# Performance work log

Hardware: AMD Instinct MI355X
Metric: run time of the kernel (lower is better)

## Reference

```python
import jax, jax.numpy as jnp
import numpy as np
import math

B, IN, D, H, DEPTH, E, K = 16384, 128, 512, 8, 3, 8, 2
FF, EH = 4 * D, 256          # ffn width = 4*d_model; expert hidden fixed at 256 in source
EPSILON = 0.1                # forward() default epsilon (exploration mixing)
LN_EPS = 1e-5


def _ln(x, w, b):
    m = x.mean(-1, keepdims=True)
    v = x.var(-1, keepdims=True)  # biased variance, matching nn.LayerNorm
    return (x - m) / jnp.sqrt(v + LN_EPS) * w + b


def setup_inputs() -> dict:
    key = jax.random.key(0)
    ks = jax.random.split(key, 16)
    s = 0.02
    rn = lambda k, shape: jax.random.normal(k, shape, jnp.float32) * s
    return dict(
        x=jax.random.normal(ks[0], (B, IN), jnp.float32),
        embed_w=rn(ks[1], (IN, D)), embed_b=jnp.zeros((D,), jnp.float32),
        ln1_w=jnp.ones((DEPTH, D), jnp.float32), ln1_b=jnp.zeros((DEPTH, D), jnp.float32),
        inproj_w=rn(ks[2], (DEPTH, 3 * D, D)), inproj_b=jnp.zeros((DEPTH, 3 * D), jnp.float32),
        outproj_w=rn(ks[3], (DEPTH, D, D)), outproj_b=jnp.zeros((DEPTH, D), jnp.float32),
        ln2_w=jnp.ones((DEPTH, D), jnp.float32), ln2_b=jnp.zeros((DEPTH, D), jnp.float32),
        ffn_w1=rn(ks[4], (DEPTH, D, FF)), ffn_b1=jnp.zeros((DEPTH, FF), jnp.float32),
        ffn_w2=rn(ks[5], (DEPTH, FF, D)), ffn_b2=jnp.zeros((DEPTH, D), jnp.float32),
        router_w=rn(ks[6], (D, E)), router_b=jnp.zeros((E,), jnp.float32),
        exp_w1=rn(ks[7], (E, D, EH)), exp_b1=jnp.zeros((E, EH), jnp.float32),
        exp_w2=rn(ks[8], (E, EH, D)), exp_b2=jnp.zeros((E, D), jnp.float32),
        head_ln_w=jnp.ones((D,), jnp.float32), head_ln_b=jnp.zeros((D,), jnp.float32),
        head_w=rn(ks[9], (D, 1)), head_b=jnp.zeros((1,), jnp.float32),
    )


def reference(x, embed_w, embed_b, ln1_w, ln1_b, inproj_w, inproj_b,
              outproj_w, outproj_b, ln2_w, ln2_b, ffn_w1, ffn_b1, ffn_w2, ffn_b2,
              router_w, router_b, exp_w1, exp_b1, exp_w2, exp_b2,
              head_ln_w, head_ln_b, head_w, head_b):
    h = x @ embed_w + embed_b                       # [B, D]; unsqueeze(1) -> seq_len == 1
    for l in range(DEPTH):
        g = _ln(h, ln1_w[l], ln1_b[l])
        qkv = g @ inproj_w[l].T + inproj_b[l]       # [B, 3D]
        # seq_len == 1: softmax over the single key is exactly 1, so attn(h,h,h) == out_proj(V)
        v = qkv[:, 2 * D:]
        a = v @ outproj_w[l].T + outproj_b[l]
        h = h + a
        g = _ln(h, ln2_w[l], ln2_b[l])
        h = h + jax.nn.gelu(g @ ffn_w1[l] + ffn_b1[l], approximate=False) @ ffn_w2[l] + ffn_b2[l]
    z = h                                           # squeeze(1)

    # WaggleGate
    logits = z @ router_w + router_b                # [B, E]
    probs = jax.nn.softmax(logits, axis=-1)
    probs = (1.0 - EPSILON) * probs + EPSILON / E
    wts, idx = jax.lax.top_k(probs, K)              # [B, K]
    load = probs.mean(0)
    aux = (load * jnp.log(load * E + 1e-9)).sum() / math.log(E + 1e-9)

    # dense all-expert compute + sparse top-k combine (same math as per-sample dispatch)
    hmid = jax.nn.gelu(jnp.einsum('bd,edh->ebh', z, exp_w1) + exp_b1[:, None, :], approximate=False)
    eo = jnp.einsum('ebh,ehd->ebd', hmid, exp_w2) + exp_b2[:, None, :]   # [E, B, D]
    gate = jnp.zeros((z.shape[0], E), z.dtype).at[
        jnp.arange(z.shape[0])[:, None], idx].add(wts)                    # [B, E]
    moe = jnp.einsum('be,ebd->bd', gate, eo)

    z = z + moe
    logit = (_ln(z, head_ln_w, head_ln_b) @ head_w + head_b)[:, 0]       # [B]
    return logit, aux
```

## Files before the change

### kernel.cpp

```cpp
#include <hip/hip_runtime.h>
#include <hip/hip_bf16.h>

#define B_TOK 16384
#define IN_DIM 128
#define D_DIM 512
#define DEPTH 3
#define NEXP 8
#define FF_DIM 2048
#define EH_DIM 256
#define MAXSLOT 34816
#define MAXT256 136
#define NHBLK 64

typedef __attribute__((ext_vector_type(8))) __bf16 bf16x8;
typedef __attribute__((ext_vector_type(4))) float f32x4;
typedef __attribute__((ext_vector_type(4))) unsigned short u16x4;
typedef __attribute__((ext_vector_type(8))) unsigned short u16x8;

__device__ __forceinline__ unsigned short f2bf(float f){
    unsigned int u = __float_as_uint(f);
    u += 0x7fffu + ((u >> 16) & 1u);
    return (unsigned short)(u >> 16);
}
__device__ __forceinline__ float bf2f(unsigned short u){
    return __uint_as_float(((unsigned int)u) << 16);
}
__device__ __forceinline__ float geluf(float x){
    float x2 = x * x;
    float y  = x * (0.79788456080287f + 0.03567740814183f * x2);
    y = fminf(fmaxf(y, -15.0f), 15.0f);
    float e = __expf(2.0f * y);
    float th = 1.0f - 2.0f / (e + 1.0f);
    return 0.5f * x * (1.0f + th);
}
__device__ __forceinline__ void gload_lds16(const void* g, void* l){
    __builtin_amdgcn_global_load_lds((const __attribute__((address_space(1))) unsigned int*)g,
                                     (__attribute__((address_space(3))) unsigned int*)l,
                                     16, 0, 0);
}
__device__ __forceinline__ int xcd_swizzle(int orig, int nwg){
    const int q = nwg >> 3, r = nwg & 7;
    const int xcd = orig & 7;
    const int idx = orig >> 3;
    return (xcd < r ? xcd*(q+1) : r*(q+1) + (xcd-r)*q) + idx;
}
__device__ __forceinline__ void wgbar(){
    asm volatile("" ::: "memory");
    __builtin_amdgcn_s_barrier();
    asm volatile("" ::: "memory");
}

__global__ void zero_kernel(int* a, int na, int* b, int nb){
    const int i = blockIdx.x * blockDim.x + threadIdx.x;
    if (i < na) a[i] = 0;
    if (i < nb) b[i] = 0;
}

struct ConvSeg { const float* src; unsigned short* dst; int n4; };
struct ConvArgs { ConvSeg seg[2]; };

__global__ void convert_kernel(ConvArgs a){
    const int stride = gridDim.x * blockDim.x;
    const int tid = blockIdx.x * blockDim.x + threadIdx.x;
    for (int s = 0; s < 2; ++s){
        const f32x4* src = (const f32x4*)a.seg[s].src;
        u16x4* dst = (u16x4*)a.seg[s].dst;
        const int n4 = a.seg[s].n4;
        for (int i = tid; i < n4; i += stride){
            f32x4 v = src[i];
            u16x4 o;
            o[0] = f2bf(v[0]); o[1] = f2bf(v[1]); o[2] = f2bf(v[2]); o[3] = f2bf(v[3]);
            dst[i] = o;
        }
    }
}

struct TSeg { const float* src; unsigned short* dst; int K; int N; int tileStart; };
struct TArgs { TSeg seg[26]; };

__global__ void transpose_kernel(TArgs a){
    __shared__ float t[32][33];
    const int tile = blockIdx.x;
    int s = 0;
    #pragma unroll 1
    while (s < 25 && tile >= a.seg[s+1].tileStart) ++s;
    const TSeg sg = a.seg[s];
    const int local = tile - sg.tileStart;
    const int tilesN = sg.N >> 5;
    const int k0 = (local / tilesN) << 5;
    const int n0 = (local % tilesN) << 5;
    const int tx = threadIdx.x & 31;
    const int ty = threadIdx.x >> 5;
    #pragma unroll
    for (int j = 0; j < 4; ++j)
        t[ty + j*8][tx] = sg.src[(size_t)(k0 + ty + j*8) * sg.N + n0 + tx];
    __syncthreads();
    #pragma unroll
    for (int j = 0; j < 4; ++j){
        const int n = ty + j*8;
        sg.dst[(size_t)(n0 + n) * sg.K + k0 + tx] = f2bf(t[tx][n]);
    }
}

__global__ void foldb_kernel(const float* __restrict__ outproj_w, const float* __restrict__ outproj_b,
                             const float* __restrict__ inproj_b, float* __restrict__ bfold){
    const int wave = threadIdx.x >> 6, lane = threadIdx.x & 63;
    const int o = blockIdx.x * 4 + wave;
    const int l = o >> 9, n = o & 511;
    const float* Wo = outproj_w + ((size_t)l*D_DIM + n)*D_DIM;
    const float* bv = inproj_b + l*3*D_DIM + 2*D_DIM;
    float s = 0.f;
    #pragma unroll
    for (int j = 0; j < 8; ++j) s += Wo[lane + j*64] * bv[lane + j*64];
    #pragma unroll
    for (int off = 32; off > 0; off >>= 1) s += __shfl_xor(s, off);
    if (lane == 0) bfold[o] = s + outproj_b[o];
}

__global__ void __launch_bounds__(256, 2)
gemm_bt(const unsigned short* __restrict__ A0, const unsigned short* __restrict__ Bt0,
        const float* __restrict__ bias, unsigned short* __restrict__ out0,
        int NB, int N, int K, int nper, size_t lsa, size_t lsb, size_t lsc)
{
    __shared__ unsigned short sh[32768];
    const int nwg = gridDim.x;
    int wg  = xcd_swizzle(blockIdx.x, nwg);
    const int layer = wg / nper;
    wg -= layer * nper;
    const unsigned short* A  = A0  + (size_t)layer * lsa;
    const unsigned short* Bt = Bt0 + (size_t)layer * lsb;
    unsigned short* out = out0 + (size_t)layer * lsc;
    const int bn  = wg % NB;
    const int bm  = wg / NB;

    const int tid  = threadIdx.x;
    const int lane = tid & 63;
    const int wave = tid >> 6;
    const int wm = (wave >> 1) << 6;
    const int wn = (wave & 1) << 6;

    f32x4 acc[4][4] = {};

    const unsigned short* Abase = A + (size_t)bm * 128 * K;
    const unsigned short* Bbase = Bt + (size_t)bn * 128 * K;
    const int soff = tid * 16;

    auto STAGE = [&](int b, int kt){
        char* Ab = (char*)(sh + b*16384);
        char* Bb = (char*)(sh + b*16384 + 8192);
        #pragma unroll
        for (int s = 0; s < 4; ++s){
            const int off = s*4096 + soff;
            const int row = off >> 7, colb = off & 127;
            gload_lds16((const char*)(Abase + (size_t)row*K + kt) + colb, Ab + off);
        }
        #pragma unroll
        for (int s = 0; s < 4; ++s){
            const int off = s*4096 + soff;
            const int row = off >> 7, colb = off & 127;
            gload_lds16((const char*)(Bbase + (size_t)row*K + kt) + colb, Bb + off);
        }
    };
    auto COMPUTE = [&](int b){
        const unsigned short* Ab = sh + b*16384;
        const unsigned short* Bb = sh + b*16384 + 8192;
        #pragma unroll
        for (int ks = 0; ks < 2; ++ks){
            const int k0 = ks*32 + ((lane>>4)<<3);
            bf16x8 af[4], bfr[4];
            #pragma unroll
            for (int i=0;i<4;i++) af[i]  = *(const bf16x8*)&Ab[(wm + i*16 + (lane&15))*64 + k0];
            #pragma unroll
            for (int j=0;j<4;j++) bfr[j] = *(const bf16x8*)&Bb[(wn + j*16 + (lane&15))*64 + k0];
            #pragma unroll
            for (int i=0;i<4;i++)
                #pragma unroll
                for (int j=0;j<4;j++)
                    acc[i][j] = __builtin_amdgcn_mfma_f32_16x16x32_bf16(af[i], bfr[j], acc[i][j], 0, 0, 0);
        }
    };

    STAGE(0, 0);
    __syncthreads();
    const int nk = K >> 6;
    int cur = 0;
    for (int i = 0; i < nk; ++i){
        if (i + 1 < nk) STAGE(cur ^ 1, (i + 1) << 6);
        COMPUTE(cur);
        __syncthreads();
        cur ^= 1;
    }

    const int r0 = ((lane>>4)<<2);
    const int cc = lane & 15;
    unsigned short* Ct = sh;
    float bcol[4];
    #pragma unroll
    for (int j=0;j<4;j++) bcol[j] = bias[bn*128 + wn + j*16 + cc];
    #pragma unroll
    for (int i=0;i<4;i++)
        #pragma unroll
        for (int r=0;r<4;r++){
            const int rl = wm + i*16 + r0 + r;
            #pragma unroll
            for (int j=0;j<4;j++)
                Ct[rl*128 + wn + j*16 + cc] = f2bf(acc[i][j][r] + bcol[j]);
        }
    __syncthreads();
    const int orow = tid >> 4;
    const int ocol = (tid & 15) * 8;
    #pragma unroll
    for (int p = 0; p < 8; ++p){
        const int row = p*16 + orow;
        *(u16x8*)(&out[(size_t)(bm*128 + row)*N + bn*128 + ocol]) = *(u16x8*)&Ct[row*128 + ocol];
    }
}

__global__ void __launch_bounds__(512, 2)
gemm256sq(const unsigned short* __restrict__ A, const unsigned short* __restrict__ Bt,
          const float* __restrict__ bias, unsigned short* __restrict__ out,
          int NB, int N, int K)
{
    __shared__ __align__(16) char sh[131072];
    const int nwg = gridDim.x;
    const int wg  = xcd_swizzle(blockIdx.x, nwg);
    const int bn  = wg % NB;
    const int bm  = wg / NB;
    const int m0  = bm * 256;
    const int n0  = bn * 256;

    const int tid = threadIdx.x, lane = tid & 63, wave = tid >> 6;
    const int wr = wave >> 2;
    const int wc = wave & 3;

    const int srow8  = tid >> 3;
    const int schunk = (tid & 7) ^ (srow8 & 7);
    const unsigned short* Ab = A  + (size_t)m0 * K + schunk*8;
    const unsigned short* Bb = Bt + (size_t)n0 * K + schunk*8;
    const int ldst = (tid & 7) * 16;

    auto STA = [&](int slot, int half, int kt){
        #pragma unroll
        for (int l = 0; l < 2; ++l){
            const int r = half*128 + srow8 + l*64;
            gload_lds16(Ab + (size_t)r*K + kt, sh + slot*32768 + r*128 + ldst);
        }
    };
    auto STB = [&](int slot, int half, int kt){
        #pragma unroll
        for (int l = 0; l < 2; ++l){
            const int r = half*128 + srow8 + l*64;
            gload_lds16(Bb + (size_t)r*K + kt, sh + 65536 + slot*32768 + r*128 + ldst);
        }
    };

    int ch[2];
    #pragma unroll
    for (int ks = 0; ks < 2; ++ks)
        ch[ks] = ((((ks<<2) + (lane>>4)) ^ (lane & 7)) << 4);
    const int arow = wr*128 + (lane & 15);
    const int brow = wc*64  + (lane & 15);

    f32x4 acc[8][4] = {};
    bf16x8 bfr[4][2];

    auto PHASE = [&](int slot, int mfb, bool rb, auto&& issue, int wait){
        if (rb){
            #pragma unroll
            for (int nf = 0; nf < 4; ++nf)
                #pragma unroll
                for (int ks = 0; ks < 2; ++ks)
                    bfr[nf][ks] = *(const bf16x8*)(sh + 65536 + slot*32768 + (brow + nf*16)*128 + ch[ks]);
        }
        bf16x8 af[2][2];
        #pragma unroll
        for (int m2 = 0; m2 < 2; ++m2)
            #pragma unroll
            for (int ks = 0; ks < 2; ++ks)
                af[m2][ks] = *(const bf16x8*)(sh + slot*32768 + (arow + (mfb+m2)*16)*128 + ch[ks]);
        issue();
        if (wait == 4)      asm volatile("s_waitcnt vmcnt(4)" ::: "memory");
        else if (wait == 0) asm volatile("s_waitcnt vmcnt(0)" ::: "memory");
        wgbar();
        __builtin_amdgcn_s_setprio(1);
        #pragma unroll
        for (int m2 = 0; m2 < 2; ++m2)
            #pragma unroll
            for (int nf = 0; nf < 4; ++nf)
                #pragma unroll
                for (int ks = 0; ks < 2; ++ks)
                    acc[mfb+m2][nf] = __builtin_amdgcn_mfma_f32_16x16x32_bf16(af[m2][ks], bfr[nf][ks], acc[mfb+m2][nf], 0,0,0);
        __builtin_amdgcn_s_setprio(0);
        wgbar();
    };

    STB(0,0,0); STB(0,1,0);
    STA(0,0,0); STA(0,1,0);
    STB(1,0,64); STB(1,1,64);
    asm volatile("s_waitcnt vmcnt(4)" ::: "memory");
    wgbar();

    const int nk = K >> 6;
    const int NT = nk >> 1;
    for (int it = 0; it < NT; ++it){
        const bool mp = (it + 1 < NT);
        const int k1 = (2*it + 1) << 6;
        const int k2 = (2*it + 2) << 6;
        const int k3 = (2*it + 3) << 6;
        PHASE(0, 0, true,  [&]{ STA(1,0,k1); }, -1);
        PHASE(0, 2, false, [&]{ STA(1,1,k1); if (mp) STB(0,0,k2); }, -1);
        PHASE(0, 4, false, [&]{ if (mp) STB(0,1,k2); }, -1);
        PHASE(0, 6, false, [&]{}, mp ? 4 : 0);
        PHASE(1, 0, true,  [&]{ if (mp) STA(0,0,k2); }, -1);
        PHASE(1, 2, false, [&]{ if (mp) STA(0,1,k2); }, -1);
        PHASE(1, 4, false, [&]{ if (mp) STB(1,0,k3); }, -1);
        PHASE(1, 6, false, [&]{ if (mp) STB(1,1,k3); }, mp ? 4 : 0);
    }

    unsigned short* Ct = (unsigned short*)sh;
    const int r4 = (lane >> 4) * 4;
    const int cc = lane & 15;
    #pragma unroll
    for (int nf = 0; nf < 4; ++nf){
        const int col = wc*64 + nf*16 + cc;
        const float bv = bias[n0 + col];
        #pragma unroll
        for (int mf = 0; mf < 8; ++mf)
            #pragma unroll
            for (int r = 0; r < 4; ++r){
                const int row = wr*128 + mf*16 + r4 + r;
                Ct[row*256 + col] = f2bf(geluf(acc[mf][nf][r] + bv));
            }
    }
    __syncthreads();
    #pragma unroll
    for (int p = 0; p < 16; ++p){
        const int uidx = p*512 + tid;
        const int row = uidx >> 5;
        const int cu  = uidx & 31;
        *(u16x8*)(out + (size_t)(m0 + row)*N + n0 + cu*8) = *(const u16x8*)(Ct + row*256 + cu*8);
    }
}

#define G_GELU_BF16 0
#define G_BF16_RESID 1
#define G_GATED_BF16 2

template<int EPI, int MOE, int INDIRECT>
__global__ void __launch_bounds__(512, 2)
gemm256(const unsigned short* __restrict__ A, const unsigned short* __restrict__ BtG,
        const float* __restrict__ biasG, const unsigned short* __restrict__ resid,
        const int* __restrict__ tok, const int* __restrict__ offs,
        int wstride, int bstride, const float* __restrict__ gslot,
        unsigned short* __restrict__ out, int NB, int N, int K)
{
    __shared__ __align__(16) char sh[147456];
    const int nwg = gridDim.x;
    const int wg  = xcd_swizzle(blockIdx.x, nwg);
    const int bn  = wg % NB;
    const int bm  = wg / NB;
    const int m0  = bm * 256;

    const unsigned short* Bt = BtG;
    const float* bias = biasG;
    if (MOE){
        if (m0 >= offs[8]) return;
        int e = 0;
        #pragma unroll 1
        while (offs[e+1] <= m0) ++e;
        Bt   += (size_t)e * wstride;
        bias += (size_t)e * bstride;
    }

    const int tid = threadIdx.x, lane = tid & 63, wave = tid >> 6;
    const int wm = (wave >> 1) * 64;
    const int wn = (wave & 1) * 64;

    const int srow = wave*16 + (lane >> 3);
    const int scol = ((lane & 7) ^ (lane >> 3)) * 8;
    const unsigned short* aptr[2][2];
    #pragma unroll
    for (int u = 0; u < 2; ++u)
        #pragma unroll
        for (int l = 0; l < 2; ++l){
            const int r = u*128 + srow + l*8;
            const int gr = INDIRECT ? tok[m0 + r] : (m0 + r);
            aptr[u][l] = A + (size_t)gr * K + scol;
        }
    const unsigned short* bptr[2];
    #pragma unroll
    for (int l = 0; l < 2; ++l)
        bptr[l] = Bt + (size_t)(bn*128 + srow + l*8) * K + scol;
    const int sdst = wave*2048 + lane*16;

    int aoff[2], boff[2];
    #pragma unroll
    for (int ks = 0; ks < 2; ++ks){
        const int ch = (((ks<<2) + (lane>>4)) ^ (lane & 7)) << 4;
        aoff[ks] = (wm + (lane & 15))*128 + ch;
        boff[ks] = (wn + (lane & 15))*128 + ch;
    }

    f32x4 acc[4][4] = {};

    auto STAGE = [&](int buf, int kt){
        #pragma unroll
        for (int u = 0; u < 2; ++u)
            #pragma unroll
            for (int l = 0; l < 2; ++l)
                gload_lds16(aptr[u][l] + kt, sh + buf*32768 + u*16384 + l*1024 + sdst);
        #pragma unroll
        for (int l = 0; l < 2; ++l)
            gload_lds16(bptr[l] + kt, sh + 98304 + buf*16384 + l*1024 + sdst);
    };
    auto COMPUTE = [&](int buf){
        bf16x8 bfr[4][2];
        #pragma unroll
        for (int nf = 0; nf < 4; ++nf)
            #pragma unroll
            for (int ks = 0; ks < 2; ++ks)
                bfr[nf][ks] = *(const bf16x8*)(sh + 98304 + buf*16384 + nf*2048 + boff[ks]);
        #pragma unroll
        for (int mf = 0; mf < 4; ++mf){
            bf16x8 af[2];
            #pragma unroll
            for (int ks = 0; ks < 2; ++ks)
                af[ks] = *(const bf16x8*)(sh + buf*32768 + mf*2048 + aoff[ks]);
            #pragma unroll
            for (int nf = 0; nf < 4; ++nf)
                #pragma unroll
                for (int ks = 0; ks < 2; ++ks)
                    acc[mf][nf] = __builtin_amdgcn_mfma_f32_16x16x32_bf16(af[ks], bfr[nf][ks], acc[mf][nf], 0,0,0);
        }
    };

    STAGE(0, 0);
    __syncthreads();
    const int nk = K >> 6;
    int cur = 0;
    for (int i = 0; i < nk; ++i){
        if (i + 1 < nk) STAGE(cur ^ 1, (i + 1) << 6);
        COMPUTE(cur);
        __syncthreads();
        cur ^= 1;
    }

    const int r4 = (lane >> 4) * 4;
    const int cc = lane & 15;
    if (EPI == G_BF16_RESID){
        float* ctf = (float*)sh;
        #pragma unroll
        for (int nf = 0; nf < 4; ++nf){
            const float bv = bias[bn*128 + wn + nf*16 + cc];
            #pragma unroll
            for (int mf = 0; mf < 4; ++mf)
                #pragma unroll
                for (int r = 0; r < 4; ++r){
                    const int row = wm + mf*16 + r4 + r;
                    ctf[row*128 + wn + nf*16 + cc] = acc[mf][nf][r] + bv;
                }
        }
        __syncthreads();
        #pragma unroll
        for (int p = 0; p < 8; ++p){
            const int uidx = p*512 + tid;
            const int row = uidx >> 4;
            const int cu  = uidx & 15;
            const size_t gidx = (size_t)(m0 + row)*N + bn*128 + cu*8;
            u16x8 hv = *(const u16x8*)(resid + gidx);
            u16x8 o;
            #pragma unroll
            for (int j = 0; j < 8; ++j)
                o[j] = f2bf(bf2f(hv[j]) + ctf[row*128 + cu*8 + j]);
            *(u16x8*)(out + gidx) = o;
        }
    } else {
        unsigned short* ct = (unsigned short*)sh;
        #pragma unroll
        for (int nf = 0; nf < 4; ++nf){
            const float bv = bias[bn*128 + wn + nf*16 + cc];
            #pragma unroll
            for (int mf = 0; mf < 4; ++mf)
                #pragma unroll
                for (int r = 0; r < 4; ++r){
                    const int row = wm + mf*16 + r4 + r;
                    float v = acc[mf][nf][r] + bv;
                    if (EPI == G_GELU_BF16) v = geluf(v);
                    else                    v *= gslot[m0 + row];
                    ct[row*128 + wn + nf*16 + cc] = f2bf(v);
                }
        }
        __syncthreads();
        #pragma unroll
        for (int p = 0; p < 8; ++p){
            const int uidx = p*512 + tid;
            const int row = uidx >> 4;
            const int cu  = uidx & 15;
            *(u16x8*)(out + (size_t)(m0 + row)*N + bn*128 + cu*8) =
                *(const u16x8*)(ct + row*128 + cu*8);
        }
    }
}

__global__ void ln_kernel(const unsigned short* __restrict__ x, const float* __restrict__ w,
                          const float* __restrict__ b, unsigned short* __restrict__ out)
{
    const int lane = threadIdx.x & 63;
    const int wave = threadIdx.x >> 6;
    const int row  = blockIdx.x * 4 + wave;
    u16x8 hv = *(const u16x8*)(x + (size_t)row * D_DIM + lane*8);
    float v[8];
    #pragma unroll
    for (int j = 0; j < 8; ++j) v[j] = bf2f(hv[j]);
    float s = 0.f, s2 = 0.f;
    #pragma unroll
    for (int j = 0; j < 8; ++j){ s += v[j]; s2 += v[j]*v[j]; }
    #pragma unroll
    for (int o = 32; o > 0; o >>= 1){ s += __shfl_xor(s, o); s2 += __shfl_xor(s2, o); }
    const float mean = s * (1.0f/512.0f);
    const float var  = s2 * (1.0f/512.0f) - mean*mean;
    const float inv  = 1.0f / sqrtf(var + 1e-5f);
    const int k = lane*8;
    u16x8 o;
    #pragma unroll
    for (int j = 0; j < 8; ++j) o[j] = f2bf((v[j]-mean)*inv*w[k+j] + b[k+j]);
    *(u16x8*)(out + (size_t)row*D_DIM + k) = o;
}

__global__ void router_kernel(const unsigned short* __restrict__ z, const float* __restrict__ rw,
                              const float* __restrict__ rb,
                              int2* __restrict__ idx2, float2* __restrict__ wts2,
                              float* __restrict__ bsums)
{
    __shared__ float ps[4][8];
    const int lane = threadIdx.x & 63;
    const int wave = threadIdx.x >> 6;
    const int row  = blockIdx.x * 4 + wave;
    u16x8 hv = *(const u16x8*)(z + (size_t)row * D_DIM + lane*8);
    float acc[8] = {0,0,0,0,0,0,0,0};
    #pragma unroll
    for (int j = 0; j < 8; ++j){
        const float zv = bf2f(hv[j]);
        const float* wr = rw + (size_t)(lane*8 + j) * 8;
        f32x4 w0 = *(const f32x4*)wr;
        f32x4 w1 = *(const f32x4*)(wr + 4);
        acc[0] += zv*w0[0]; acc[1] += zv*w0[1]; acc[2] += zv*w0[2]; acc[3] += zv*w0[3];
        acc[4] += zv*w1[0]; acc[5] += zv*w1[1]; acc[6] += zv*w1[2]; acc[7] += zv*w1[3];
    }
    #pragma unroll
    for (int o = 32; o > 0; o >>= 1){
        #pragma unroll
        for (int e = 0; e < 8; ++e) acc[e] += __shfl_xor(acc[e], o);
    }
    if (lane == 0){
        float p[8]; float mx = -1e30f;
        #pragma unroll
        for (int e=0;e<8;e++){ p[e] = acc[e] + rb[e]; mx = fmaxf(mx, p[e]); }
        float se = 0.f;
        #pragma unroll
        for (int e=0;e<8;e++){ p[e] = expf(p[e]-mx); se += p[e]; }
        const float sc = 0.9f / se;
        #pragma unroll
        for (int e=0;e<8;e++) p[e] = p[e]*sc + 0.0125f;
        int i1 = 0;
        #pragma unroll
        for (int e=1;e<8;e++) if (p[e] > p[i1]) i1 = e;
        int i2 = (i1 == 0) ? 1 : 0;
        for (int e=i2+1;e<8;e++) if (e != i1 && p[e] > p[i2]) i2 = e;
        idx2[row] = make_int2(i1, i2);
        wts2[row] = make_float2(p[i1], p[i2]);
        #pragma unroll
        for (int e=0;e<8;e++) ps[wave][e] = p[e];
    }
    __syncthreads();
    if (threadIdx.x < 8){
        bsums[blockIdx.x*8 + threadIdx.x] =
            ps[0][threadIdx.x] + ps[1][threadIdx.x] + ps[2][threadIdx.x] + ps[3][threadIdx.x];
    }
}

__global__ void hist_kernel(const int2* __restrict__ idx2, int* __restrict__ blockHist){
    __shared__ int hc[8];
    if (threadIdx.x < 8) hc[threadIdx.x] = 0;
    __syncthreads();
    const int t = blockIdx.x * 256 + threadIdx.x;
    const int2 ii = idx2[t];
    atomicAdd(&hc[ii.x], 1);
    atomicAdd(&hc[ii.y], 1);
    __syncthreads();
    if (threadIdx.x < 8) blockHist[blockIdx.x*8 + threadIdx.x] = hc[threadIdx.x];
}

__global__ void scan_kernel(const int* __restrict__ blockHist, int* __restrict__ offs,
                            int* __restrict__ baseArr){
    __shared__ int hist[NHBLK*8];
    __shared__ int cnt[8];
    __shared__ int start[8];
    const int t = threadIdx.x;
    hist[t] = blockHist[t];
    __syncthreads();
    if (t < 8){
        int c = 0;
        #pragma unroll 1
        for (int b = 0; b < NHBLK; ++b) c += hist[b*8 + t];
        cnt[t] = c;
    }
    __syncthreads();
    if (t == 0){
        int o = 0; offs[0] = 0;
        for (int e = 0; e < 8; ++e){ start[e] = o; o += (cnt[e]+255)&~255; offs[e+1] = o; }
    }
    __syncthreads();
    if (t < 8){
        int cur = start[t];
        #pragma unroll 1
        for (int b = 0; b < NHBLK; ++b){ baseArr[b*8 + t] = cur; cur += hist[b*8 + t]; }
    }
}

__global__ void assign_kernel(const int2* __restrict__ idx2, const float2* __restrict__ wts2,
                              const int* __restrict__ baseArr, int2* __restrict__ slot_map,
                              float* __restrict__ gslot, int* __restrict__ tok)
{
    __shared__ int cur[8];
    if (threadIdx.x < 8) cur[threadIdx.x] = 0;
    __syncthreads();
    const int t = blockIdx.x * 256 + threadIdx.x;
    const int2 ii = idx2[t];
    const float2 ww = wts2[t];
    const int r1 = atomicAdd(&cur[ii.x], 1);
    const int r2 = atomicAdd(&cur[ii.y], 1);
    const int s1 = baseArr[blockIdx.x*8 + ii.x] + r1;
    const int s2 = baseArr[blockIdx.x*8 + ii.y] + r2;
    slot_map[t] = make_int2(s1, s2);
    gslot[s1] = ww.x; gslot[s2] = ww.y;
    tok[s1] = t; tok[s2] = t;
}

__global__ void aux_kernel(const float* __restrict__ bsums, float* __restrict__ out_aux)
{
    __shared__ float part[256];
    const int t = threadIdx.x;
    const int e = t & 7, chunk = t >> 3;
    float s = 0.f;
    for (int blk = chunk*128; blk < chunk*128 + 128; ++blk) s += bsums[blk*8 + e];
    part[t] = s;
    __syncthreads();
    if (t < 8){
        float tot = 0.f;
        for (int c = 0; c < 32; ++c) tot += part[c*8 + t];
        part[t] = tot;
    }
    __syncthreads();
    if (t == 0){
        float aux = 0.f;
        for (int e2 = 0; e2 < 8; ++e2){
            float load = part[e2] * (1.0f/16384.0f);
            aux += load * logf(load * 8.0f + 1e-9f);
        }
        out_aux[0] = aux / 2.0794415416798357f;
    }
}

__global__ void head_kernel(const unsigned short* __restrict__ h, const unsigned short* __restrict__ eog,
                            const int2* __restrict__ slot_map,
                            const float* __restrict__ w, const float* __restrict__ b,
                            const float* __restrict__ hw, const float* __restrict__ hb,
                            float* __restrict__ out)
{
    const int lane = threadIdx.x & 63;
    const int wave = threadIdx.x >> 6;
    const int row  = blockIdx.x * 4 + wave;
    const int2 sm = slot_map[row];
    u16x8 hv = *(const u16x8*)(h + (size_t)row * D_DIM + lane*8);
    u16x8 e1 = *(const u16x8*)(eog + (size_t)sm.x * D_DIM + lane*8);
    u16x8 e2 = *(const u16x8*)(eog + (size_t)sm.y * D_DIM + lane*8);
    float v[8];
    #pragma unroll
    for (int j=0;j<8;j++) v[j] = bf2f(hv[j]) + bf2f(e1[j]) + bf2f(e2[j]);
    float s = 0.f, s2 = 0.f;
    #pragma unroll
    for (int j=0;j<8;j++){ s += v[j]; s2 += v[j]*v[j]; }
    #pragma unroll
    for (int o = 32; o > 0; o >>= 1){ s += __shfl_xor(s, o); s2 += __shfl_xor(s2, o); }
    const float mean = s * (1.0f/512.0f);
    const float var  = s2 * (1.0f/512.0f) - mean*mean;
    const float inv  = 1.0f / sqrtf(var + 1e-5f);
    const int k = lane*8;
    float dot = 0.f;
    #pragma unroll
    for (int j=0;j<8;j++) dot += ((v[j]-mean)*inv*w[k+j] + b[k+j]) * hw[k+j];
    #pragma unroll
    for (int o = 32; o > 0; o >>= 1) dot += __shfl_xor(dot, o);
    if (lane == 0) out[row] = dot + hb[0];
}

extern "C" void kernel_launch(void* const* d_in, const int* in_sizes, int n_in,
                              void* d_out, int out_size, void* d_ws, size_t ws_size,
                              hipStream_t stream)
{
    (void)in_sizes; (void)n_in; (void)out_size; (void)ws_size;
    const float* x         = (const float*)d_in[0];
    const float* embed_w   = (const float*)d_in[1];
    const float* embed_b   = (const float*)d_in[2];
    const float* ln1_w     = (const float*)d_in[3];
    const float* ln1_b     = (const float*)d_in[4];
    const float* inproj_w  = (const float*)d_in[5];
    const float* inproj_b  = (const float*)d_in[6];
    const float* outproj_w = (const float*)d_in[7];
    const float* outproj_b = (const float*)d_in[8];
    const float* ln2_w     = (const float*)d_in[9];
    const float* ln2_b     = (const float*)d_in[10];
    const float* ffn_w1    = (const float*)d_in[11];
    const float* ffn_b1    = (const float*)d_in[12];
    const float* ffn_w2    = (const float*)d_in[13];
    const float* ffn_b2    = (const float*)d_in[14];
    const float* router_w  = (const float*)d_in[15];
    const float* router_b  = (const float*)d_in[16];
    const float* exp_w1    = (const float*)d_in[17];
    const float* exp_b1    = (const float*)d_in[18];
    const float* exp_w2    = (const float*)d_in[19];
    const float* exp_b2    = (const float*)d_in[20];
    const float* head_ln_w = (const float*)d_in[21];
    const float* head_ln_b = (const float*)d_in[22];
    const float* head_w    = (const float*)d_in[23];
    const float* head_b    = (const float*)d_in[24];

    char* ws = (char*)d_ws;
    unsigned short* xbf   = (unsigned short*)(ws + 0);
    unsigned short* ebf   = (unsigned short*)(ws + 4194304);
    unsigned short* wobf  = (unsigned short*)(ws + 4325376);
    unsigned short* wvtbf = (unsigned short*)(ws + 5898240);
    unsigned short* wfold = (unsigned short*)(ws + 7471104);
    unsigned short* w1t   = (unsigned short*)(ws + 9043968);
    unsigned short* w2t   = (unsigned short*)(ws + 15335424);
    unsigned short* e1t   = (unsigned short*)(ws + 21626880);
    unsigned short* e2t   = (unsigned short*)(ws + 23724032);
    unsigned short* h     = (unsigned short*)(ws + 25821184);
    unsigned short* gbf   = (unsigned short*)(ws + 42598400);
    unsigned short* ubf   = (unsigned short*)(ws + 59375616);
    unsigned short* hmidg = ubf;
    unsigned short* eog   = (unsigned short*)(ws + 77201408);
    char* MISC = ws + 126484480;
    int*    offs     = (int*)(MISC + 0);
    float*  zbias    = (float*)(MISC + 256);
    float*  bfold    = (float*)(MISC + 2304);
    int2*   idx2     = (int2*)(MISC + 8448);
    float2* wts2     = (float2*)(MISC + 139520);
    int2*   slot_map = (int2*)(MISC + 270592);
    float*  gslot    = (float*)(MISC + 401664);
    int*    tok      = (int*)(MISC + 544768);
    float*  bsums    = (float*)(MISC + 684032);
    int*    blockHist= (int*)(MISC + 815104);
    int*    baseArr  = (int*)(MISC + 817152);
    float* out = (float*)d_out;

    zero_kernel<<<(MAXSLOT + 255)/256, 256, 0, stream>>>((int*)zbias, 512, tok, MAXSLOT);

    ConvArgs ca;
    ca.seg[0] = { x, xbf, B_TOK*IN_DIM/4 };
    ca.seg[1] = { outproj_w, wobf, DEPTH*D_DIM*D_DIM/4 };
    convert_kernel<<<1024, 256, 0, stream>>>(ca);

    TArgs ta;
    int tcur = 0, ti = 0;
    ta.seg[ti] = { embed_w, ebf, IN_DIM, D_DIM, tcur };
    tcur += (IN_DIM/32)*(D_DIM/32); ++ti;
    for (int l = 0; l < DEPTH; ++l){
        ta.seg[ti] = { ffn_w1 + (size_t)l*D_DIM*FF_DIM, w1t + (size_t)l*FF_DIM*D_DIM, D_DIM, FF_DIM, tcur };
        tcur += (D_DIM/32)*(FF_DIM/32); ++ti;
    }
    for (int l = 0; l < DEPTH; ++l){
        ta.seg[ti] = { ffn_w2 + (size_t)l*FF_DIM*D_DIM, w2t + (size_t)l*D_DIM*FF_DIM, FF_DIM, D_DIM, tcur };
        tcur += (FF_DIM/32)*(D_DIM/32); ++ti;
    }
    for (int e = 0; e < NEXP; ++e){
        ta.seg[ti] = { exp_w1 + (size_t)e*D_DIM*EH_DIM, e1t + (size_t)e*EH_DIM*D_DIM, D_DIM, EH_DIM, tcur };
        tcur += (D_DIM/32)*(EH_DIM/32); ++ti;
    }
    for (int e = 0; e < NEXP; ++e){
        ta.seg[ti] = { exp_w2 + (size_t)e*EH_DIM*D_DIM, e2t + (size_t)e*D_DIM*EH_DIM, EH_DIM, D_DIM, tcur };
        tcur += (EH_DIM/32)*(D_DIM/32); ++ti;
    }
    for (int l = 0; l < DEPTH; ++l){
        ta.seg[ti] = { inproj_w + (size_t)l*3*D_DIM*D_DIM + 2*D_DIM*D_DIM,
                       wvtbf + (size_t)l*D_DIM*D_DIM, D_DIM, D_DIM, tcur };
        tcur += (D_DIM/32)*(D_DIM/32); ++ti;
    }
    transpose_kernel<<<tcur, 256, 0, stream>>>(ta);

    foldb_kernel<<<DEPTH*D_DIM/4, 256, 0, stream>>>(outproj_w, outproj_b, inproj_b, bfold);

    gemm_bt<<<48, 256, 0, stream>>>(
        wobf, wvtbf, zbias, wfold, 4, D_DIM, D_DIM,
        16, (size_t)D_DIM*D_DIM, (size_t)D_DIM*D_DIM, (size_t)D_DIM*D_DIM);

    gemm_bt<<<(D_DIM/128)*(B_TOK/128), 256, 0, stream>>>(
        xbf, ebf, embed_b, h, D_DIM/128, D_DIM, IN_DIM,
        (D_DIM/128)*(B_TOK/128), 0, 0, 0);

    for (int l = 0; l < DEPTH; ++l){
        ln_kernel<<<B_TOK/4, 256, 0, stream>>>(h, ln1_w + l*D_DIM, ln1_b + l*D_DIM, gbf);
        gemm256<G_BF16_RESID,0,0><<<(B_TOK/256)*(D_DIM/128), 512, 0, stream>>>(
            gbf, wfold + (size_t)l*D_DIM*D_DIM, bfold + l*D_DIM, h,
            nullptr, nullptr, 0, 0, nullptr, h, D_DIM/128, D_DIM, D_DIM);
        ln_kernel<<<B_TOK/4, 256, 0, stream>>>(h, ln2_w + l*D_DIM, ln2_b + l*D_DIM, gbf);
        gemm256sq<<<(B_TOK/256)*(FF_DIM/256), 512, 0, stream>>>(
            gbf, w1t + (size_t)l*FF_DIM*D_DIM, ffn_b1 + l*FF_DIM, ubf, FF_DIM/256, FF_DIM, D_DIM);
        gemm256<G_BF16_RESID,0,0><<<(B_TOK/256)*(D_DIM/128), 512, 0, stream>>>(
            ubf, w2t + (size_t)l*D_DIM*FF_DIM, ffn_b2 + l*D_DIM, h,
            nullptr, nullptr, 0, 0, nullptr, h, D_DIM/128, D_DIM, FF_DIM);
    }

    router_kernel<<<B_TOK/4, 256, 0, stream>>>(h, router_w, router_b, idx2, wts2, bsums);
    aux_kernel<<<1, 256, 0, stream>>>(bsums, out + B_TOK);
    hist_kernel<<<NHBLK, 256, 0, stream>>>(idx2, blockHist);
    scan_kernel<<<1, 512, 0, stream>>>(blockHist, offs, baseArr);
    assign_kernel<<<B_TOK/256, 256, 0, stream>>>(idx2, wts2, baseArr, slot_map, gslot, tok);

    gemm256<G_GELU_BF16,1,1><<<MAXT256*(EH_DIM/128), 512, 0, stream>>>(
        h, e1t, exp_b1, nullptr, tok, offs, EH_DIM*D_DIM, EH_DIM, nullptr,
        hmidg, EH_DIM/128, EH_DIM, D_DIM);
    gemm256<G_GATED_BF16,1,0><<<MAXT256*(D_DIM/128), 512, 0, stream>>>(
        hmidg, e2t, exp_b2, nullptr, nullptr, offs, D_DIM*EH_DIM, D_DIM, gslot,
        eog, D_DIM/128, D_DIM, EH_DIM);

    head_kernel<<<B_TOK/4, 256, 0, stream>>>(h, eog, slot_map, head_ln_w, head_ln_b, head_w, head_b, out);
}
```

Measured before the change: 571.0 us.

## Halve GEMM K-tile to 32 to cut LDS footprint and raise occupancy

Both the 256x256 GELU GEMM and the generic 256x128 GEMM now stage K-tiles of 32 instead of 64, which shrinks shared memory from 128-144KB to 64KB per workgroup. The 256-square kernel also drops its hand-scheduled eight-phase pipeline with interleaved barriers and priority hints, and uses a plain double-buffered loop. Epilogues are split into two 128-row halves so the output staging fits in the smaller LDS. The aim is more resident workgroups per CU and simpler scheduling, at the cost of twice as many barriers per K and less latency hiding within each workgroup.

```diff
diff --git a/kernel.cpp b/kernel.cpp
--- a/kernel.cpp
+++ b/kernel.cpp
@@ -43,11 +43,6 @@
     const int xcd = orig & 7;
     const int idx = orig >> 3;
     return (xcd < r ? xcd*(q+1) : r*(q+1) + (xcd-r)*q) + idx;
-}
-__device__ __forceinline__ void wgbar(){
-    asm volatile("" ::: "memory");
-    __builtin_amdgcn_s_barrier();
-    asm volatile("" ::: "memory");
 }
 
 __global__ void zero_kernel(int* a, int na, int* b, int nb){
@@ -221,7 +216,7 @@
           const float* __restrict__ bias, unsigned short* __restrict__ out,
           int NB, int N, int K)
 {
-    __shared__ __align__(16) char sh[131072];
+    __shared__ __align__(16) char sh[65536];
     const int nwg = gridDim.x;
     const int wg  = xcd_swizzle(blockIdx.x, nwg);
     const int bn  = wg % NB;
@@ -233,112 +228,86 @@
     const int wr = wave >> 2;
     const int wc = wave & 3;
 
-    const int srow8  = tid >> 3;
-    const int schunk = (tid & 7) ^ (srow8 & 7);
-    const unsigned short* Ab = A  + (size_t)m0 * K + schunk*8;
-    const unsigned short* Bb = Bt + (size_t)n0 * K + schunk*8;
-    const int ldst = (tid & 7) * 16;
-
-    auto STA = [&](int slot, int half, int kt){
-        #pragma unroll
-        for (int l = 0; l < 2; ++l){
-            const int r = half*128 + srow8 + l*64;
-            gload_lds16(Ab + (size_t)r*K + kt, sh + slot*32768 + r*128 + ldst);
-        }
+    const unsigned short* apt[2]; int adst[2];
+    const unsigned short* bpt[2];
+    #pragma unroll
+    for (int l = 0; l < 2; ++l){
+        const int slot = l*512 + tid;
+        const int row = slot >> 2, ch = slot & 3;
+        const int srccol = ((ch ^ (row & 3)) << 3);
+        apt[l]  = A  + (size_t)(m0 + row)*K + srccol;
+        bpt[l]  = Bt + (size_t)(n0 + row)*K + srccol;
+        adst[l] = row*64 + ch*16;
+    }
+    auto STAGE = [&](int buf, int kt){
+        #pragma unroll
+        for (int l = 0; l < 2; ++l)
+            gload_lds16(apt[l] + kt, sh + buf*16384 + adst[l]);
+        #pragma unroll
+        for (int l = 0; l < 2; ++l)
+            gload_lds16(bpt[l] + kt, sh + 32768 + buf*16384 + adst[l]);
     };
-    auto STB = [&](int slot, int half, int kt){
-        #pragma unroll
-        for (int l = 0; l < 2; ++l){
-            const int r = half*128 + srow8 + l*64;
-            gload_lds16(Bb + (size_t)r*K + kt, sh + 65536 + slot*32768 + r*128 + ldst);
-        }
-    };
-
-    int ch[2];
-    #pragma unroll
-    for (int ks = 0; ks < 2; ++ks)
-        ch[ks] = ((((ks<<2) + (lane>>4)) ^ (lane & 7)) << 4);
+
+    const int rch  = (((lane>>4) ^ (lane & 3)) << 4);
     const int arow = wr*128 + (lane & 15);
     const int brow = wc*64  + (lane & 15);
 
     f32x4 acc[8][4] = {};
-    bf16x8 bfr[4][2];
-
-    auto PHASE = [&](int slot, int mfb, bool rb, auto&& issue, int wait){
-        if (rb){
+
+    auto COMPUTE = [&](int buf){
+        bf16x8 bfr[4];
+        #pragma unroll
+        for (int nf = 0; nf < 4; ++nf)
+            bfr[nf] = *(const bf16x8*)(sh + 32768 + buf*16384 + (brow + nf*16)*64 + rch);
+        #pragma unroll
+        for (int mf = 0; mf < 8; ++mf){
+            bf16x8 af = *(const bf16x8*)(sh + buf*16384 + (arow + mf*16)*64 + rch);
             #pragma unroll
             for (int nf = 0; nf < 4; ++nf)
-                #pragma unroll
-                for (int ks = 0; ks < 2; ++ks)
-                    bfr[nf][ks] = *(const bf16x8*)(sh + 65536 + slot*32768 + (brow + nf*16)*128 + ch[ks]);
-        }
-        bf16x8 af[2][2];
-        #pragma unroll
-        for (int m2 = 0; m2 < 2; ++m2)
-            #pragma unroll
-            for (int ks = 0; ks < 2; ++ks)
-                af[m2][ks] = *(const bf16x8*)(sh + slot*32768 + (arow + (mfb+m2)*16)*128 + ch[ks]);
-        issue();
-        if (wait == 4)      asm volatile("s_waitcnt vmcnt(4)" ::: "memory");
-        else if (wait == 0) asm volatile("s_waitcnt vmcnt(0)" ::: "memory");
-        wgbar();
-        __builtin_amdgcn_s_setprio(1);
-        #pragma unroll
-        for (int m2 = 0; m2 < 2; ++m2)
-            #pragma unroll
-            for (int nf = 0; nf < 4; ++nf)
-                #pragma unroll
-                for (int ks = 0; ks < 2; ++ks)
-                    acc[mfb+m2][nf] = __builtin_amdgcn_mfma_f32_16x16x32_bf16(af[m2][ks], bfr[nf][ks], acc[mfb+m2][nf], 0,0,0);
-        __builtin_amdgcn_s_setprio(0);
-        wgbar();
+                acc[mf][nf] = __builtin_amdgcn_mfma_f32_16x16x32_bf16(af, bfr[nf], acc[mf][nf], 0,0,0);
+        }
     };
 
-    STB(0,0,0); STB(0,1,0);
-    STA(0,0,0); STA(0,1,0);
-    STB(1,0,64); STB(1,1,64);
-    asm volatile("s_waitcnt vmcnt(4)" ::: "memory");
-    wgbar();
-
-    const int nk = K >> 6;
-    const int NT = nk >> 1;
-    for (int it = 0; it < NT; ++it){
-        const bool mp = (it + 1 < NT);
-        const int k1 = (2*it + 1) << 6;
-        const int k2 = (2*it + 2) << 6;
-        const int k3 = (2*it + 3) << 6;
-        PHASE(0, 0, true,  [&]{ STA(1,0,k1); }, -1);
-        PHASE(0, 2, false, [&]{ STA(1,1,k1); if (mp) STB(0,0,k2); }, -1);
-        PHASE(0, 4, false, [&]{ if (mp) STB(0,1,k2); }, -1);
-        PHASE(0, 6, false, [&]{}, mp ? 4 : 0);
-        PHASE(1, 0, true,  [&]{ if (mp) STA(0,0,k2); }, -1);
-        PHASE(1, 2, false, [&]{ if (mp) STA(0,1,k2); }, -1);
-        PHASE(1, 4, false, [&]{ if (mp) STB(1,0,k3); }, -1);
-        PHASE(1, 6, false, [&]{ if (mp) STB(1,1,k3); }, mp ? 4 : 0);
+    STAGE(0, 0);
+    __syncthreads();
+    const int nk = K >> 5;
+    int cur = 0;
+    for (int i = 0; i < nk; ++i){
+        if (i + 1 < nk) STAGE(cur ^ 1, (i + 1) << 5);
+        COMPUTE(cur);
+        __syncthreads();
+        cur ^= 1;
     }
 
     unsigned short* Ct = (unsigned short*)sh;
     const int r4 = (lane >> 4) * 4;
     const int cc = lane & 15;
-    #pragma unroll
-    for (int nf = 0; nf < 4; ++nf){
-        const int col = wc*64 + nf*16 + cc;
-        const float bv = bias[n0 + col];
-        #pragma unroll
-        for (int mf = 0; mf < 8; ++mf)
-            #pragma unroll
-            for (int r = 0; r < 4; ++r){
-                const int row = wr*128 + mf*16 + r4 + r;
-                Ct[row*256 + col] = f2bf(geluf(acc[mf][nf][r] + bv));
+    float bcol[4];
+    #pragma unroll
+    for (int nf = 0; nf < 4; ++nf) bcol[nf] = bias[n0 + wc*64 + nf*16 + cc];
+    #pragma unroll
+    for (int half = 0; half < 2; ++half){
+        if (wr == half){
+            #pragma unroll
+            for (int nf = 0; nf < 4; ++nf){
+                const int col = wc*64 + nf*16 + cc;
+                #pragma unroll
+                for (int mf = 0; mf < 8; ++mf)
+                    #pragma unroll
+                    for (int r = 0; r < 4; ++r)
+                        Ct[(mf*16 + r4 + r)*256 + col] = f2bf(geluf(acc[mf][nf][r] + bcol[nf]));
             }
-    }
-    __syncthreads();
-    #pragma unroll
-    for (int p = 0; p < 16; ++p){
-        const int uidx = p*512 + tid;
-        const int row = uidx >> 5;
-        const int cu  = uidx & 31;
-        *(u16x8*)(out + (size_t)(m0 + row)*N + n0 + cu*8) = *(const u16x8*)(Ct + row*256 + cu*8);
+        }
+        __syncthreads();
+        #pragma unroll
+        for (int p = 0; p < 8; ++p){
+            const int uidx = p*512 + tid;
+            const int row = uidx >> 5;
+            const int cu  = uidx & 31;
+            *(u16x8*)(out + (size_t)(m0 + half*128 + row)*N + n0 + cu*8) =
+                *(const u16x8*)(Ct + row*256 + cu*8);
+        }
+        __syncthreads();
     }
 }
 
@@ -354,7 +323,7 @@
         int wstride, int bstride, const float* __restrict__ gslot,
         unsigned short* __restrict__ out, int NB, int N, int K)
 {
-    __shared__ __align__(16) char sh[147456];
+    __shared__ __align__(16) char sh[65536];
     const int nwg = gridDim.x;
     const int wg  = xcd_swizzle(blockIdx.x, nwg);
     const int bn  = wg % NB;
@@ -376,70 +345,56 @@
     const int wm = (wave >> 1) * 64;
     const int wn = (wave & 1) * 64;
 
-    const int srow = wave*16 + (lane >> 3);
-    const int scol = ((lane & 7) ^ (lane >> 3)) * 8;
-    const unsigned short* aptr[2][2];
-    #pragma unroll
-    for (int u = 0; u < 2; ++u)
-        #pragma unroll
-        for (int l = 0; l < 2; ++l){
-            const int r = u*128 + srow + l*8;
-            const int gr = INDIRECT ? tok[m0 + r] : (m0 + r);
-            aptr[u][l] = A + (size_t)gr * K + scol;
-        }
-    const unsigned short* bptr[2];
-    #pragma unroll
-    for (int l = 0; l < 2; ++l)
-        bptr[l] = Bt + (size_t)(bn*128 + srow + l*8) * K + scol;
-    const int sdst = wave*2048 + lane*16;
-
-    int aoff[2], boff[2];
-    #pragma unroll
-    for (int ks = 0; ks < 2; ++ks){
-        const int ch = (((ks<<2) + (lane>>4)) ^ (lane & 7)) << 4;
-        aoff[ks] = (wm + (lane & 15))*128 + ch;
-        boff[ks] = (wn + (lane & 15))*128 + ch;
-    }
+    const unsigned short* apt[2]; int adst[2];
+    #pragma unroll
+    for (int l = 0; l < 2; ++l){
+        const int slot = l*512 + tid;
+        const int row = slot >> 2, ch = slot & 3;
+        const int srccol = ((ch ^ (row & 3)) << 3);
+        const int gr = INDIRECT ? tok[m0 + row] : (m0 + row);
+        apt[l]  = A + (size_t)gr*K + srccol;
+        adst[l] = row*64 + ch*16;
+    }
+    const unsigned short* bpt; int bdst;
+    {
+        const int row = tid >> 2, ch = tid & 3;
+        const int srccol = ((ch ^ (row & 3)) << 3);
+        bpt  = Bt + (size_t)(bn*128 + row)*K + srccol;
+        bdst = row*64 + ch*16;
+    }
+    auto STAGE = [&](int buf, int kt){
+        #pragma unroll
+        for (int l = 0; l < 2; ++l)
+            gload_lds16(apt[l] + kt, sh + buf*16384 + adst[l]);
+        gload_lds16(bpt + kt, sh + 32768 + buf*8192 + bdst);
+    };
+
+    const int rch  = (((lane>>4) ^ (lane & 3)) << 4);
+    const int arow = wm + (lane & 15);
+    const int brow = wn + (lane & 15);
 
     f32x4 acc[4][4] = {};
 
-    auto STAGE = [&](int buf, int kt){
-        #pragma unroll
-        for (int u = 0; u < 2; ++u)
-            #pragma unroll
-            for (int l = 0; l < 2; ++l)
-                gload_lds16(aptr[u][l] + kt, sh + buf*32768 + u*16384 + l*1024 + sdst);
-        #pragma unroll
-        for (int l = 0; l < 2; ++l)
-            gload_lds16(bptr[l] + kt, sh + 98304 + buf*16384 + l*1024 + sdst);
+    auto COMPUTE = [&](int buf){
+        bf16x8 bfr[4];
+        #pragma unroll
+        for (int nf = 0; nf < 4; ++nf)
+            bfr[nf] = *(const bf16x8*)(sh + 32768 + buf*8192 + (brow + nf*16)*64 + rch);
+        #pragma unroll
+        for (int mf = 0; mf < 4; ++mf){
+            bf16x8 af = *(const bf16x8*)(sh + buf*16384 + (arow + mf*16)*64 + rch);
+            #pragma unroll
+            for (int nf = 0; nf < 4; ++nf)
+                acc[mf][nf] = __builtin_amdgcn_mfma_f32_16x16x32_bf16(af, bfr[nf], acc[mf][nf], 0,0,0);
+        }
     };
-    auto COMPUTE = [&](int buf){
-        bf16x8 bfr[4][2];
-        #pragma unroll
-        for (int nf = 0; nf < 4; ++nf)
-            #pragma unroll
-            for (int ks = 0; ks < 2; ++ks)
-                bfr[nf][ks] = *(const bf16x8*)(sh + 98304 + buf*16384 + nf*2048 + boff[ks]);
-        #pragma unroll
-        for (int mf = 0; mf < 4; ++mf){
-            bf16x8 af[2];
-            #pragma unroll
-            for (int ks = 0; ks < 2; ++ks)
-                af[ks] = *(const bf16x8*)(sh + buf*32768 + mf*2048 + aoff[ks]);
-            #pragma unroll
-            for (int nf = 0; nf < 4; ++nf)
-                #pragma unroll
-                for (int ks = 0; ks < 2; ++ks)
-                    acc[mf][nf] = __builtin_amdgcn_mfma_f32_16x16x32_bf16(af[ks], bfr[nf][ks], acc[mf][nf], 0,0,0);
-        }
-    };
 
     STAGE(0, 0);
     __syncthreads();
-    const int nk = K >> 6;
+    const int nk = K >> 5;
     int cur = 0;
     for (int i = 0; i < nk; ++i){
-        if (i + 1 < nk) STAGE(cur ^ 1, (i + 1) << 6);
+        if (i + 1 < nk) STAGE(cur ^ 1, (i + 1) << 5);
         COMPUTE(cur);
         __syncthreads();
         cur ^= 1;
@@ -449,42 +404,50 @@
     const int cc = lane & 15;
     if (EPI == G_BF16_RESID){
         float* ctf = (float*)sh;
+        float bcol[4];
+        #pragma unroll
+        for (int nf = 0; nf < 4; ++nf) bcol[nf] = bias[bn*128 + wn + nf*16 + cc];
+        #pragma unroll
+        for (int half = 0; half < 2; ++half){
+            if ((wm >> 7) == half){
+                const int wml = wm & 127;
+                #pragma unroll
+                for (int nf = 0; nf < 4; ++nf)
+                    #pragma unroll
+                    for (int mf = 0; mf < 4; ++mf)
+                        #pragma unroll
+                        for (int r = 0; r < 4; ++r)
+                            ctf[(wml + mf*16 + r4 + r)*128 + wn + nf*16 + cc] = acc[mf][nf][r] + bcol[nf];
+            }
+            __syncthreads();
+            #pragma unroll
+            for (int p = 0; p < 4; ++p){
+                const int uidx = p*512 + tid;
+                const int row = uidx >> 4;
+                const int cu  = uidx & 15;
+                const size_t gidx = (size_t)(m0 + half*128 + row)*N + bn*128 + cu*8;
+                u16x8 hv = *(const u16x8*)(resid + gidx);
+                u16x8 o;
+                #pragma unroll
+                for (int j = 0; j < 8; ++j)
+                    o[j] = f2bf(bf2f(hv[j]) + ctf[row*128 + cu*8 + j]);
+                *(u16x8*)(out + gidx) = o;
+            }
+            __syncthreads();
+        }
+    } else {
+        unsigned short* ct = (unsigned short*)sh;
+        float bcol[4];
+        #pragma unroll
+        for (int nf = 0; nf < 4; ++nf) bcol[nf] = bias[bn*128 + wn + nf*16 + cc];
         #pragma unroll
         for (int nf = 0; nf < 4; ++nf){
-            const float bv = bias[bn*128 + wn + nf*16 + cc];
             #pragma unroll
             for (int mf = 0; mf < 4; ++mf)
                 #pragma unroll
                 for (int r = 0; r < 4; ++r){
                     const int row = wm + mf*16 + r4 + r;
-                    ctf[row*128 + wn + nf*16 + cc] = acc[mf][nf][r] + bv;
-                }
-        }
-        __syncthreads();
-        #pragma unroll
-        for (int p = 0; p < 8; ++p){
-            const int uidx = p*512 + tid;
-            const int row = uidx >> 4;
-            const int cu  = uidx & 15;
-            const size_t gidx = (size_t)(m0 + row)*N + bn*128 + cu*8;
-            u16x8 hv = *(const u16x8*)(resid + gidx);
-            u16x8 o;
-            #pragma unroll
-            for (int j = 0; j < 8; ++j)
-                o[j] = f2bf(bf2f(hv[j]) + ctf[row*128 + cu*8 + j]);
-            *(u16x8*)(out + gidx) = o;
-        }
-    } else {
-        unsigned short* ct = (unsigned short*)sh;
-        #pragma unroll
-        for (int nf = 0; nf < 4; ++nf){
-            const float bv = bias[bn*128 + wn + nf*16 + cc];
-            #pragma unroll
-            for (int mf = 0; mf < 4; ++mf)
-                #pragma unroll
-                for (int r = 0; r < 4; ++r){
-                    const int row = wm + mf*16 + r4 + r;
-                    float v = acc[mf][nf][r] + bv;
+                    float v = acc[mf][nf][r] + bcol[nf];
                     if (EPI == G_GELU_BF16) v = geluf(v);
                     else                    v *= gslot[m0 + row];
                     ct[row*128 + wn + nf*16 + cc] = f2bf(v);
```

After: 644.0 us. 12.8% more time.
